# Performance work log

Hardware: AMD Instinct MI355X
Metric: run time of the kernel (lower is better)

Reference implementation:

```python
import jax, jax.numpy as jnp
import numpy as np

N = 100000   # nodes
E = 1600000  # edges (avg degree 16)
F = 64       # in_feats
H = 128      # hidden_size
O = 10       # out_feats
L = 3        # SAGEConv layers
EPS = 1e-5


def setup_inputs() -> dict:
    key = jax.random.key(0)
    ks = jax.random.split(key, 16)
    s = 0.05
    return {
        "nodes": jax.random.normal(ks[0], (N, F), jnp.float32),
        "src": jax.random.randint(ks[1], (E,), 0, N),
        "dst": jax.random.randint(ks[2], (E,), 0, N),
        # input MLP: Linear(F,H) -> ReLU -> Linear(H,H)
        "W_in1": jax.random.normal(ks[3], (F, H), jnp.float32) * s,
        "b_in1": jnp.zeros((H,), jnp.float32),
        "W_in2": jax.random.normal(ks[4], (H, H), jnp.float32) * s,
        "b_in2": jnp.zeros((H,), jnp.float32),
        # L stacked SAGEConv layers (mean aggregator)
        "W_self": jax.random.normal(ks[5], (L, H, H), jnp.float32) * s,
        "W_neigh": jax.random.normal(ks[6], (L, H, H), jnp.float32) * s,
        "b_sage": jnp.zeros((L, H), jnp.float32),
        "ln_g": jnp.ones((L, H), jnp.float32),
        "ln_b": jnp.zeros((L, H), jnp.float32),
        # output head Linear(H, O)
        "W_out": jax.random.normal(ks[7], (H, O), jnp.float32) * s,
        "b_out": jnp.zeros((O,), jnp.float32),
    }


def reference(nodes, src, dst, W_in1, b_in1, W_in2, b_in2,
              W_self, W_neigh, b_sage, ln_g, ln_b, W_out, b_out):
    # input MLP
    h = jax.nn.relu(nodes @ W_in1 + b_in1) @ W_in2 + b_in2  # [N, H]

    # in-degree for mean aggregation (0-degree nodes get 0 neighbor feature)
    deg = jax.ops.segment_sum(jnp.ones((E,), h.dtype), dst, num_segments=N)
    inv_deg = (1.0 / jnp.maximum(deg, 1.0))[:, None]  # [N, 1]

    for l in range(L):
        # mean over incoming neighbors: gather src feats, scatter-add to dst
        agg = jax.ops.segment_sum(h[src], dst, num_segments=N) * inv_deg  # [N, H]
        h = h @ W_self[l] + agg @ W_neigh[l] + b_sage[l]
        h = jax.nn.relu(h)
        # LayerNorm over feature dim
        mu = h.mean(-1, keepdims=True)
        var = h.var(-1, keepdims=True)
        h = ln_g[l] * (h - mu) * jax.lax.rsqrt(var + EPS) + ln_b[l]

    # dgl.mean_nodes over the single graph -> [1, H]
    g = h.mean(0, keepdims=True)
    return g @ W_out + b_out  # [1, O]
```

## Files before the change

kernel.cpp:

```cpp
#include <hip/hip_runtime.h>
#include <hip/hip_bf16.h>

#define NN 100000
#define NE 1600000
#define FF 64
#define HH 128
#define OO 10
#define NL 3
#define NB 391
#define NBLK 250
#define CHUNK 6400
#define BCAP 5376
#define LNEPS 1e-5f

typedef short s8v __attribute__((ext_vector_type(8)));
typedef float f32x4 __attribute__((ext_vector_type(4)));
typedef float f32x2 __attribute__((ext_vector_type(2)));

__device__ __forceinline__ unsigned short f2b(float f){
  unsigned u = __float_as_uint(f);
  unsigned r = (u + 0x7FFFu + ((u>>16)&1u)) >> 16;
  return (unsigned short)r;
}
__device__ __forceinline__ float b2f(unsigned short b){
  return __uint_as_float(((unsigned)b)<<16);
}

#if __has_builtin(__builtin_amdgcn_cvt_pk_f32_fp8) && __has_builtin(__builtin_amdgcn_cvt_pk_fp8_f32)
__device__ __forceinline__ unsigned char f8enc(float x){
  int p = __builtin_amdgcn_cvt_pk_fp8_f32(x, x, 0, false);
  return (unsigned char)(p & 0xFF);
}
__device__ __forceinline__ void f8dec4(unsigned u, float* o){
  f32x2 lo = __builtin_amdgcn_cvt_pk_f32_fp8(u, false);
  f32x2 hi = __builtin_amdgcn_cvt_pk_f32_fp8(u, true);
  o[0]=lo[0]; o[1]=lo[1]; o[2]=hi[0]; o[3]=hi[1];
}
#else
#include <hip/hip_fp8.h>
__device__ __forceinline__ unsigned char f8enc(float x){
  __hip_fp8_e4m3 q(x); return (unsigned char)q.__x;
}
__device__ __forceinline__ void f8dec4(unsigned u, float* o){
  for(int i=0;i<4;i++){
    __hip_fp8_e4m3 q; q.__x = (unsigned char)(u>>(8*i));
    o[i] = (float)q;
  }
}
#endif

__global__ __launch_bounds__(256) void k_bcount(const int* __restrict__ dst, int* __restrict__ bcnt,
                                                int* __restrict__ blockcnt){
  __shared__ int h[NB];
  for(int i=threadIdx.x;i<NB;i+=256) h[i]=0;
  __syncthreads();
  int base = blockIdx.x*CHUNK;
  for(int i=threadIdx.x;i<CHUNK;i+=256){
    int e = base+i;
    if(e<NE) atomicAdd(&h[((unsigned)dst[e])>>8],1);
  }
  __syncthreads();
  for(int i=threadIdx.x;i<NB;i+=256){
    int v=h[i];
    blockcnt[i*256 + blockIdx.x] = v;
    if(v) atomicAdd(&bcnt[i],v);
  }
}

__global__ void k_bscan(const int* __restrict__ bcnt, int* __restrict__ boff, int* __restrict__ rowoff){
  __shared__ int s[512];
  int t=threadIdx.x;
  int v = (t<NB)? bcnt[t]:0;
  s[t]=v; __syncthreads();
  for(int off=1;off<512;off<<=1){
    int x=(t>=off)?s[t-off]:0;
    __syncthreads();
    s[t]+=x;
    __syncthreads();
  }
  if(t<NB) boff[t]=s[t]-v;
  if(t==0) rowoff[NN]=NE;
}

__global__ void k_prefix(const int* __restrict__ blockcnt, const int* __restrict__ boff,
                         int* __restrict__ pref){
  __shared__ int s[256];
  int k=blockIdx.x, t=threadIdx.x;
  int v = (t<NBLK)? blockcnt[k*256+t] : 0;
  s[t]=v; __syncthreads();
  for(int off=1;off<256;off<<=1){
    int x=(t>=off)?s[t-off]:0;
    __syncthreads();
    s[t]+=x;
    __syncthreads();
  }
  if(t<NBLK) pref[k*256+t] = boff[k] + s[t]-v;
}

__global__ __launch_bounds__(256) void k_bscatter(const int* __restrict__ src, const int* __restrict__ dst,
                                                  const int* __restrict__ pref, unsigned* __restrict__ ebuf){
  __shared__ int cur[NB];
  __shared__ int pb[NB];
  for(int i=threadIdx.x;i<NB;i+=256){ cur[i]=0; pb[i]=pref[i*256+blockIdx.x]; }
  __syncthreads();
  int base=blockIdx.x*CHUNK;
  for(int i=threadIdx.x;i<CHUNK;i+=256){
    int e=base+i;
    if(e<NE){
      int d=dst[e];
      int k=((unsigned)d)>>8;
      int r=atomicAdd(&cur[k],1);
      ebuf[pb[k]+r] = (unsigned)src[e] | ((unsigned)(d&255)<<20);
    }
  }
}

__global__ __launch_bounds__(256) void k_bsort(const unsigned* __restrict__ ebuf, const int* __restrict__ bcnt,
                                               const int* __restrict__ boff, int* __restrict__ rowoff,
                                               float* __restrict__ invd, int* __restrict__ csr){
  __shared__ unsigned el[BCAP];
  __shared__ int dg[256], sc[256], cu[256];
  int b=blockIdx.x, t=threadIdx.x;
  int c = bcnt[b]; if(c>BCAP) c=BCAP;
  int base = boff[b];
  for(int i=t;i<c;i+=256) el[i]=ebuf[base+i];
  dg[t]=0;
  __syncthreads();
  for(int i=t;i<c;i+=256) atomicAdd(&dg[el[i]>>20],1);
  __syncthreads();
  int v = dg[t];
  sc[t]=v; __syncthreads();
  for(int off=1;off<256;off<<=1){
    int x=(t>=off)?sc[t-off]:0;
    __syncthreads();
    sc[t]+=x;
    __syncthreads();
  }
  int excl = sc[t]-v;
  int node = b*256+t;
  if(node<NN){
    rowoff[node]=base+excl;
    invd[node]=1.0f/fmaxf((float)v,1.0f);
  }
  cu[t]=excl;
  __syncthreads();
  for(int i=t;i<c;i+=256){
    unsigned e=el[i];
    int d=e>>20;
    int p=atomicAdd(&cu[d],1);
    csr[base+p] = (int)(e & 0xFFFFFu);
  }
}

__global__ void k_cvtin(const float* __restrict__ x, unsigned* __restrict__ xb, int n4){
  int i = blockIdx.x*256+threadIdx.x;
  if(i<n4){
    float4 v = *(const float4*)&x[i*4];
    uint2 p;
    p.x = (unsigned)f2b(v.x) | ((unsigned)f2b(v.y)<<16);
    p.y = (unsigned)f2b(v.z) | ((unsigned)f2b(v.w)<<16);
    *(uint2*)&xb[i*2] = p;
  }
}

__global__ void k_repack(const float* __restrict__ W1, const float* __restrict__ W2,
                         const float* __restrict__ Ws, const float* __restrict__ Wn,
                         unsigned short* __restrict__ wf){
  int t = blockIdx.x*256+threadIdx.x;
  if(t >= 122880) return;
  const float* src; int rem;
  if(t < 8192){ src = W1; rem = t; }
  else {
    int u = t - 8192;
    int m = u >> 14; rem = u & 16383;
    if(m==0) src = W2;
    else if(m<=3) src = Ws + (size_t)(m-1)*HH*HH;
    else src = Wn + (size_t)(m-4)*HH*HH;
  }
  int j = rem&7, l=(rem>>3)&63, nt=(rem>>9)&7, kcb=rem>>12;
  int k = kcb*32 + 8*(l>>4) + j;
  int n = nt*16 + (l&15);
  wf[t] = f2b(src[(size_t)k*HH + n]);
}

__global__ __launch_bounds__(256) void k_agg(const unsigned* __restrict__ hf8, const int* __restrict__ csr,
                                             const int* __restrict__ rowoff, const float* __restrict__ invd,
                                             unsigned* __restrict__ aggb){
  int wave=threadIdx.x>>6, lane=threadIdx.x&63;
  int n = blockIdx.x*4+wave;
  if(n>=NN) return;
  int beg=rowoff[n], end=rowoff[n+1];
  int c = lane&31, half=lane>>5;
  float a0=0.f,a1=0.f,a2=0.f,a3=0.f;
  int j=beg;
  for(; j+4<=end; j+=4){
    int s0=csr[j+half], s1=csr[j+2+half];
    unsigned u0=hf8[(size_t)s0*32+c], u1=hf8[(size_t)s1*32+c];
    float d0[4], d1[4];
    f8dec4(u0,d0); f8dec4(u1,d1);
    a0+=d0[0]+d1[0]; a1+=d0[1]+d1[1]; a2+=d0[2]+d1[2]; a3+=d0[3]+d1[3];
  }
  for(; j+2<=end; j+=2){
    int s0=csr[j+half];
    unsigned u0=hf8[(size_t)s0*32+c];
    float d0[4];
    f8dec4(u0,d0);
    a0+=d0[0]; a1+=d0[1]; a2+=d0[2]; a3+=d0[3];
  }
  if(j<end && half==0){
    int s0=csr[j];
    unsigned u0=hf8[(size_t)s0*32+c];
    float d0[4];
    f8dec4(u0,d0);
    a0+=d0[0]; a1+=d0[1]; a2+=d0[2]; a3+=d0[3];
  }
  a0+=__shfl_xor(a0,32); a1+=__shfl_xor(a1,32);
  a2+=__shfl_xor(a2,32); a3+=__shfl_xor(a3,32);
  if(half==0){
    float s=invd[n];
    uint2 p;
    p.x = (unsigned)f2b(a0*s) | ((unsigned)f2b(a1*s)<<16);
    p.y = (unsigned)f2b(a2*s) | ((unsigned)f2b(a3*s)<<16);
    *(uint2*)&aggb[(size_t)n*64 + 2*c] = p;
  }
}

template<int K, int DUAL, int RELU, int LN, int F8>
__global__ __launch_bounds__(256) void k_mfma(
    const unsigned short* __restrict__ A, const unsigned short* __restrict__ A2,
    const unsigned short* __restrict__ Wf, const unsigned short* __restrict__ Wf2,
    const float* __restrict__ bias, const float* __restrict__ lng, const float* __restrict__ lnb,
    unsigned short* __restrict__ out, unsigned char* __restrict__ hf8)
{
  constexpr int KC = K/32;
  __shared__ unsigned short Wl[KC*8*64*8];
  __shared__ unsigned short Wl2[DUAL ? KC*8*64*8 : 8];
  int tid = threadIdx.x;
  {
    const int tot = KC*8*64*8/8;
    for(int i=tid;i<tot;i+=256){
      ((uint4*)Wl)[i] = ((const uint4*)Wf)[i];
      if(DUAL) ((uint4*)Wl2)[i] = ((const uint4*)Wf2)[i];
    }
  }
  __syncthreads();
  int l = tid&63, wv = tid>>6;
  int grp = l>>4, lc = l&15;
  int node0 = blockIdx.x*64 + wv*16;
  int arow = node0 + lc; if(arow > NN-1) arow = NN-1;
  f32x4 acc[8] = {};
  const s8v* Wv  = (const s8v*)Wl;
  const s8v* Wv2 = (const s8v*)Wl2;
  #pragma unroll
  for(int kcb=0;kcb<KC;kcb++){
    s8v a = *(const s8v*)&A[(size_t)arow*K + kcb*32 + 8*grp];
    s8v a2;
    if(DUAL) a2 = *(const s8v*)&A2[(size_t)arow*K + kcb*32 + 8*grp];
    #pragma unroll
    for(int nt=0;nt<8;nt++){
      acc[nt] = __builtin_amdgcn_mfma_f32_16x16x32_bf16(a, Wv[(kcb*8+nt)*64 + l], acc[nt], 0,0,0);
      if(DUAL)
        acc[nt] = __builtin_amdgcn_mfma_f32_16x16x32_bf16(a2, Wv2[(kcb*8+nt)*64 + l], acc[nt], 0,0,0);
    }
  }
  float bc[8], gc[8], oc[8];
  #pragma unroll
  for(int nt=0;nt<8;nt++){
    bc[nt] = bias[nt*16+lc];
    if(LN){ gc[nt]=lng[nt*16+lc]; oc[nt]=lnb[nt*16+lc]; }
  }
  #pragma unroll
  for(int r=0;r<4;r++){
    float x[8]; float s=0.f, ss=0.f;
    #pragma unroll
    for(int nt=0;nt<8;nt++){
      float v = acc[nt][r] + bc[nt];
      if(RELU) v = fmaxf(v, 0.f);
      x[nt]=v; s+=v; ss+=v*v;
    }
    if(LN){
      #pragma unroll
      for(int m=1;m<=8;m<<=1){ s+=__shfl_xor(s,m); ss+=__shfl_xor(ss,m); }
      float mu = s*(1.0f/HH);
      float var = ss*(1.0f/HH) - mu*mu;
      float rs = rsqrtf(var + LNEPS);
      #pragma unroll
      for(int nt=0;nt<8;nt++) x[nt] = gc[nt]*(x[nt]-mu)*rs + oc[nt];
    }
    int node = node0 + grp*4 + r;
    if(node<NN){
      #pragma unroll
      for(int nt=0;nt<8;nt++) out[(size_t)node*HH + nt*16 + lc] = f2b(x[nt]);
      if(F8){
        #pragma unroll
        for(int nt=0;nt<8;nt++) hf8[(size_t)node*HH + nt*16 + lc] = f8enc(x[nt]);
      }
    }
  }
}

__global__ void k_mean(const unsigned short* __restrict__ hb, float* __restrict__ g){
  int col=threadIdx.x;
  float s=0.f;
  for(int n=blockIdx.x; n<NN; n+=gridDim.x) s += b2f(hb[(size_t)n*HH + col]);
  atomicAdd(&g[col], s);
}

__global__ void k_out(const float* __restrict__ g, const float* __restrict__ Wout,
                      const float* __restrict__ bout, float* __restrict__ out){
  int o=threadIdx.x;
  if(o<OO){
    float acc=bout[o];
    for(int k=0;k<HH;k++) acc = fmaf(g[k]*(1.0f/NN), Wout[k*OO+o], acc);
    out[o]=acc;
  }
}

extern "C" void kernel_launch(void* const* d_in, const int* in_sizes, int n_in,
                              void* d_out, int out_size, void* d_ws, size_t ws_size,
                              hipStream_t stream){
  const float* nodes = (const float*)d_in[0];
  const int*   src   = (const int*)d_in[1];
  const int*   dst   = (const int*)d_in[2];
  const float* W_in1 = (const float*)d_in[3];
  const float* b_in1 = (const float*)d_in[4];
  const float* W_in2 = (const float*)d_in[5];
  const float* b_in2 = (const float*)d_in[6];
  const float* W_self  = (const float*)d_in[7];
  const float* W_neigh = (const float*)d_in[8];
  const float* b_sage  = (const float*)d_in[9];
  const float* ln_g    = (const float*)d_in[10];
  const float* ln_b    = (const float*)d_in[11];
  const float* W_out   = (const float*)d_in[12];
  const float* b_out   = (const float*)d_in[13];

  char* w=(char*)d_ws;
  unsigned short* hb   = (unsigned short*)w; w += (size_t)NN*HH*2;
  unsigned short* aggb = (unsigned short*)w; w += (size_t)NN*HH*2;
  unsigned short* xb   = (unsigned short*)w; w += (size_t)NN*FF*2;
  unsigned char*  hf8  = (unsigned char*)w;  w += (size_t)NN*HH;
  unsigned short* wf   = (unsigned short*)w; w += (size_t)122880*2;
  unsigned* ebuf = (unsigned*)w; w += (size_t)NE*4;
  int* csr    = (int*)w;   w += (size_t)NE*4;
  int* rowoff = (int*)w;   w += (size_t)(NN+8)*4;
  float* invd = (float*)w; w += (size_t)NN*4;
  int* bcnt   = (int*)w;   w += (size_t)(NB+1)*4;
  int* boff   = (int*)w;   w += (size_t)(NB+1)*4;
  int* blockcnt=(int*)w;   w += (size_t)NB*256*4;
  int* pref   = (int*)w;   w += (size_t)NB*256*4;
  float* gsum = (float*)w; w += 128*4;

  hipMemsetAsync(bcnt, 0, (size_t)(NB+1)*4, stream);
  hipMemsetAsync(gsum, 0, 128*4, stream);

  k_bcount<<<NBLK,256,0,stream>>>(dst,bcnt,blockcnt);
  k_bscan<<<1,512,0,stream>>>(bcnt,boff,rowoff);
  k_prefix<<<NB,256,0,stream>>>(blockcnt,boff,pref);
  k_bscatter<<<NBLK,256,0,stream>>>(src,dst,pref,ebuf);
  k_bsort<<<NB,256,0,stream>>>(ebuf,bcnt,boff,rowoff,invd,csr);

  k_cvtin<<<((NN*FF/4)+255)/256,256,0,stream>>>(nodes,(unsigned*)xb, NN*FF/4);
  k_repack<<<(122880+255)/256,256,0,stream>>>(W_in1,W_in2,W_self,W_neigh,wf);

  const int GB = (NN+63)/64;
  k_mfma<FF,0,1,0,0><<<GB,256,0,stream>>>(xb,nullptr, wf, nullptr, b_in1,nullptr,nullptr, aggb, nullptr);
  k_mfma<HH,0,0,0,1><<<GB,256,0,stream>>>(aggb,nullptr, wf+8192, nullptr, b_in2,nullptr,nullptr, hb, hf8);

  for(int l=0;l<NL;l++){
    k_agg<<<(NN+3)/4,256,0,stream>>>((const unsigned*)hf8,csr,rowoff,invd,(unsigned*)aggb);
    if(l<NL-1)
      k_mfma<HH,1,1,1,1><<<GB,256,0,stream>>>(hb, aggb,
          wf+24576+(size_t)l*16384, wf+73728+(size_t)l*16384,
          b_sage+(size_t)l*HH, ln_g+(size_t)l*HH, ln_b+(size_t)l*HH, hb, hf8);
    else
      k_mfma<HH,1,1,1,0><<<GB,256,0,stream>>>(hb, aggb,
          wf+24576+(size_t)l*16384, wf+73728+(size_t)l*16384,
          b_sage+(size_t)l*HH, ln_g+(size_t)l*HH, ln_b+(size_t)l*HH, hb, nullptr);
  }
  k_mean<<<256,128,0,stream>>>(hb,gsum);
  k_out<<<1,64,0,stream>>>(gsum,W_out,b_out,(float*)d_out);
}
```

Measured before the change: 470.7 us.

## Fuse node mean into last SAGE layer and widen fp8 gathers in aggregation

The final SAGE layer kernel now reduces its LayerNorm output per block (shuffles plus shared memory) and atomically adds it into the global column sums. This removes the bf16 write of the last hidden state and the separate mean kernel that re-read it. The aggregation kernel now has each lane load 8 fp8 values (uint2) and covers four edges per iteration across lane quarters, then finishes with two shuffle rounds and a 16-byte store. In exchange it adds block-level atomics on one shared 128-float buffer and more accumulator registers per lane.

After: 404.2 us. -14.1%, faster.

```diff
diff --git a/kernel.cpp b/kernel.cpp
--- a/kernel.cpp
+++ b/kernel.cpp
@@ -183,58 +183,60 @@
   wf[t] = f2b(src[(size_t)k*HH + n]);
 }
 
-__global__ __launch_bounds__(256) void k_agg(const unsigned* __restrict__ hf8, const int* __restrict__ csr,
+__global__ __launch_bounds__(256) void k_agg(const uint2* __restrict__ hf8, const int* __restrict__ csr,
                                              const int* __restrict__ rowoff, const float* __restrict__ invd,
-                                             unsigned* __restrict__ aggb){
+                                             uint4* __restrict__ aggb){
   int wave=threadIdx.x>>6, lane=threadIdx.x&63;
   int n = blockIdx.x*4+wave;
   if(n>=NN) return;
   int beg=rowoff[n], end=rowoff[n+1];
-  int c = lane&31, half=lane>>5;
-  float a0=0.f,a1=0.f,a2=0.f,a3=0.f;
+  int c = lane&15, q=lane>>4;
+  float a0=0.f,a1=0.f,a2=0.f,a3=0.f,a4=0.f,a5=0.f,a6=0.f,a7=0.f;
   int j=beg;
   for(; j+4<=end; j+=4){
-    int s0=csr[j+half], s1=csr[j+2+half];
-    unsigned u0=hf8[(size_t)s0*32+c], u1=hf8[(size_t)s1*32+c];
+    int s0=csr[j+q];
+    uint2 u=hf8[(size_t)s0*16+c];
     float d0[4], d1[4];
-    f8dec4(u0,d0); f8dec4(u1,d1);
-    a0+=d0[0]+d1[0]; a1+=d0[1]+d1[1]; a2+=d0[2]+d1[2]; a3+=d0[3]+d1[3];
-  }
-  for(; j+2<=end; j+=2){
-    int s0=csr[j+half];
-    unsigned u0=hf8[(size_t)s0*32+c];
-    float d0[4];
-    f8dec4(u0,d0);
+    f8dec4(u.x,d0); f8dec4(u.y,d1);
     a0+=d0[0]; a1+=d0[1]; a2+=d0[2]; a3+=d0[3];
-  }
-  if(j<end && half==0){
-    int s0=csr[j];
-    unsigned u0=hf8[(size_t)s0*32+c];
-    float d0[4];
-    f8dec4(u0,d0);
-    a0+=d0[0]; a1+=d0[1]; a2+=d0[2]; a3+=d0[3];
-  }
-  a0+=__shfl_xor(a0,32); a1+=__shfl_xor(a1,32);
-  a2+=__shfl_xor(a2,32); a3+=__shfl_xor(a3,32);
-  if(half==0){
+    a4+=d1[0]; a5+=d1[1]; a6+=d1[2]; a7+=d1[3];
+  }
+  if(j<end){
+    if(j+q<end){
+      int s0=csr[j+q];
+      uint2 u=hf8[(size_t)s0*16+c];
+      float d0[4], d1[4];
+      f8dec4(u.x,d0); f8dec4(u.y,d1);
+      a0+=d0[0]; a1+=d0[1]; a2+=d0[2]; a3+=d0[3];
+      a4+=d1[0]; a5+=d1[1]; a6+=d1[2]; a7+=d1[3];
+    }
+  }
+  a0+=__shfl_xor(a0,16); a1+=__shfl_xor(a1,16); a2+=__shfl_xor(a2,16); a3+=__shfl_xor(a3,16);
+  a4+=__shfl_xor(a4,16); a5+=__shfl_xor(a5,16); a6+=__shfl_xor(a6,16); a7+=__shfl_xor(a7,16);
+  a0+=__shfl_xor(a0,32); a1+=__shfl_xor(a1,32); a2+=__shfl_xor(a2,32); a3+=__shfl_xor(a3,32);
+  a4+=__shfl_xor(a4,32); a5+=__shfl_xor(a5,32); a6+=__shfl_xor(a6,32); a7+=__shfl_xor(a7,32);
+  if(q==0){
     float s=invd[n];
-    uint2 p;
+    uint4 p;
     p.x = (unsigned)f2b(a0*s) | ((unsigned)f2b(a1*s)<<16);
     p.y = (unsigned)f2b(a2*s) | ((unsigned)f2b(a3*s)<<16);
-    *(uint2*)&aggb[(size_t)n*64 + 2*c] = p;
-  }
-}
-
-template<int K, int DUAL, int RELU, int LN, int F8>
+    p.z = (unsigned)f2b(a4*s) | ((unsigned)f2b(a5*s)<<16);
+    p.w = (unsigned)f2b(a6*s) | ((unsigned)f2b(a7*s)<<16);
+    aggb[(size_t)n*16 + c] = p;
+  }
+}
+
+template<int K, int DUAL, int RELU, int LN, int F8, int MEAN>
 __global__ __launch_bounds__(256) void k_mfma(
     const unsigned short* __restrict__ A, const unsigned short* __restrict__ A2,
     const unsigned short* __restrict__ Wf, const unsigned short* __restrict__ Wf2,
     const float* __restrict__ bias, const float* __restrict__ lng, const float* __restrict__ lnb,
-    unsigned short* __restrict__ out, unsigned char* __restrict__ hf8)
+    unsigned short* __restrict__ out, unsigned char* __restrict__ hf8, float* __restrict__ gsum)
 {
   constexpr int KC = K/32;
   __shared__ unsigned short Wl[KC*8*64*8];
   __shared__ unsigned short Wl2[DUAL ? KC*8*64*8 : 8];
+  __shared__ float sm[MEAN ? 4*128 : 4];
   int tid = threadIdx.x;
   {
     const int tot = KC*8*64*8/8;
@@ -269,6 +271,9 @@
     bc[nt] = bias[nt*16+lc];
     if(LN){ gc[nt]=lng[nt*16+lc]; oc[nt]=lnb[nt*16+lc]; }
   }
+  float msum[8];
+  #pragma unroll
+  for(int nt=0;nt<8;nt++) msum[nt]=0.f;
   #pragma unroll
   for(int r=0;r<4;r++){
     float x[8]; float s=0.f, ss=0.f;
@@ -289,21 +294,35 @@
     }
     int node = node0 + grp*4 + r;
     if(node<NN){
+      if(MEAN){
+        #pragma unroll
+        for(int nt=0;nt<8;nt++) msum[nt]+=x[nt];
+      } else {
+        #pragma unroll
+        for(int nt=0;nt<8;nt++) out[(size_t)node*HH + nt*16 + lc] = f2b(x[nt]);
+        if(F8){
+          #pragma unroll
+          for(int nt=0;nt<8;nt++) hf8[(size_t)node*HH + nt*16 + lc] = f8enc(x[nt]);
+        }
+      }
+    }
+  }
+  if(MEAN){
+    #pragma unroll
+    for(int nt=0;nt<8;nt++){
+      msum[nt]+=__shfl_xor(msum[nt],16);
+      msum[nt]+=__shfl_xor(msum[nt],32);
+    }
+    if(grp==0){
       #pragma unroll
-      for(int nt=0;nt<8;nt++) out[(size_t)node*HH + nt*16 + lc] = f2b(x[nt]);
-      if(F8){
-        #pragma unroll
-        for(int nt=0;nt<8;nt++) hf8[(size_t)node*HH + nt*16 + lc] = f8enc(x[nt]);
-      }
-    }
-  }
-}
-
-__global__ void k_mean(const unsigned short* __restrict__ hb, float* __restrict__ g){
-  int col=threadIdx.x;
-  float s=0.f;
-  for(int n=blockIdx.x; n<NN; n+=gridDim.x) s += b2f(hb[(size_t)n*HH + col]);
-  atomicAdd(&g[col], s);
+      for(int nt=0;nt<8;nt++) sm[wv*128 + nt*16 + lc] = msum[nt];
+    }
+    __syncthreads();
+    if(tid<128){
+      float v = sm[tid] + sm[128+tid] + sm[256+tid] + sm[384+tid];
+      atomicAdd(&gsum[tid], v);
+    }
+  }
 }
 
 __global__ void k_out(const float* __restrict__ g, const float* __restrict__ Wout,
@@ -363,20 +382,19 @@
   k_repack<<<(122880+255)/256,256,0,stream>>>(W_in1,W_in2,W_self,W_neigh,wf);
 
   const int GB = (NN+63)/64;
-  k_mfma<FF,0,1,0,0><<<GB,256,0,stream>>>(xb,nullptr, wf, nullptr, b_in1,nullptr,nullptr, aggb, nullptr);
-  k_mfma<HH,0,0,0,1><<<GB,256,0,stream>>>(aggb,nullptr, wf+8192, nullptr, b_in2,nullptr,nullptr, hb, hf8);
+  k_mfma<FF,0,1,0,0,0><<<GB,256,0,stream>>>(xb,nullptr, wf, nullptr, b_in1,nullptr,nullptr, aggb, nullptr, nullptr);
+  k_mfma<HH,0,0,0,1,0><<<GB,256,0,stream>>>(aggb,nullptr, wf+8192, nullptr, b_in2,nullptr,nullptr, hb, hf8, nullptr);
 
   for(int l=0;l<NL;l++){
-    k_agg<<<(NN+3)/4,256,0,stream>>>((const unsigned*)hf8,csr,rowoff,invd,(unsigned*)aggb);
+    k_agg<<<(NN+3)/4,256,0,stream>>>((const uint2*)hf8,csr,rowoff,invd,(uint4*)aggb);
     if(l<NL-1)
-      k_mfma<HH,1,1,1,1><<<GB,256,0,stream>>>(hb, aggb,
+      k_mfma<HH,1,1,1,1,0><<<GB,256,0,stream>>>(hb, aggb,
           wf+24576+(size_t)l*16384, wf+73728+(size_t)l*16384,
-          b_sage+(size_t)l*HH, ln_g+(size_t)l*HH, ln_b+(size_t)l*HH, hb, hf8);
+          b_sage+(size_t)l*HH, ln_g+(size_t)l*HH, ln_b+(size_t)l*HH, hb, hf8, nullptr);
     else
-      k_mfma<HH,1,1,1,0><<<GB,256,0,stream>>>(hb, aggb,
+      k_mfma<HH,1,1,1,0,1><<<GB,256,0,stream>>>(hb, aggb,
           wf+24576+(size_t)l*16384, wf+73728+(size_t)l*16384,
-          b_sage+(size_t)l*HH, ln_g+(size_t)l*HH, ln_b+(size_t)l*HH, hb, nullptr);
-  }
-  k_mean<<<256,128,0,stream>>>(hb,gsum);
+          b_sage+(size_t)l*HH, ln_g+(size_t)l*HH, ln_b+(size_t)l*HH, hb, nullptr, gsum);
+  }
   k_out<<<1,64,0,stream>>>(gsum,W_out,b_out,(float*)d_out);
 }
```
